# Kernel optimization log

Measured on AMD Instinct MI355X. Metric: run time of the kernel, lower is better.

Reference implementation:

```python
import jax, jax.numpy as jnp
import numpy as np

N_NODES = 100000
N_EDGES = 3200000
IN_C, HID_C, OUT_C = 64, 64, 32


def setup_inputs() -> dict:
    key = jax.random.key(0)
    ks = jax.random.split(key, 8)
    x = jax.random.normal(ks[0], (N_NODES, IN_C), dtype=jnp.float32)
    edge_index = jax.random.randint(ks[1], (2, N_EDGES), 0, N_NODES, dtype=jnp.int64)
    s1 = 1.0 / np.sqrt(IN_C)
    s2 = 1.0 / np.sqrt(HID_C)
    W1l = jax.random.uniform(ks[2], (IN_C, HID_C), jnp.float32, -s1, s1)
    b1l = jnp.zeros((HID_C,), jnp.float32)
    W1r = jax.random.uniform(ks[3], (IN_C, HID_C), jnp.float32, -s1, s1)
    W2l = jax.random.uniform(ks[4], (HID_C, OUT_C), jnp.float32, -s2, s2)
    b2l = jnp.zeros((OUT_C,), jnp.float32)
    W2r = jax.random.uniform(ks[5], (HID_C, OUT_C), jnp.float32, -s2, s2)
    return {"x": x, "edge_index": edge_index, "W1l": W1l, "b1l": b1l,
            "W1r": W1r, "W2l": W2l, "b2l": b2l, "W2r": W2r}


def _sage_conv(x, src, dst, Wl, bl, Wr):
    # mean-aggregate source features onto destination nodes
    msg = x[src]                                              # [E, d] gather
    summed = jax.ops.segment_sum(msg, dst, num_segments=N_NODES)
    deg = jax.ops.segment_sum(jnp.ones((src.shape[0],), x.dtype), dst,
                              num_segments=N_NODES)
    agg = summed / jnp.maximum(deg, 1.0)[:, None]             # [N, d]
    return agg @ Wl + bl + x @ Wr                             # lin_l(agg)+lin_r(x)


def reference(x, edge_index, W1l, b1l, W1r, W2l, b2l, W2r):
    src, dst = edge_index[0], edge_index[1]
    h = jax.nn.relu(_sage_conv(x, src, dst, W1l, b1l, W1r))
    # dropout is identity in eval mode
    return _sage_conv(h, src, dst, W2l, b2l, W2r)
```

## Files before the change

### kernel.cpp

```cpp
#include <hip/hip_runtime.h>
#include <hip/hip_bf16.h>

#define N_NODES 100000
#define N_EDGES 3200000
#define NBKT 391
#define BKT_CAP 10240

typedef __hip_bfloat16 bf16;
typedef unsigned int uint;
typedef __attribute__((ext_vector_type(8))) short bf16x8;
typedef __attribute__((ext_vector_type(4))) float f32x4;

__device__ __forceinline__ float b2f(bf16 v) { return __bfloat162float(v); }

__device__ __forceinline__ float bits2f(unsigned short w) {
    union { unsigned short u; bf16 b; } c;
    c.u = w;
    return __bfloat162float(c.b);
}
__device__ __forceinline__ unsigned short f2bits(float f) {
    return (unsigned short)(__float_as_uint(f) >> 16);
}
__device__ __forceinline__ unsigned short f2bf_bits(float f) {
    bf16 b = __float2bfloat16(f);
    unsigned short u;
    __builtin_memcpy(&u, &b, 2);
    return u;
}

__device__ __forceinline__ int get_idx(const void* ei, long long pos, int is64) {
    if (is64) return (int)((const long long*)ei)[pos];
    return ((const int*)ei)[pos];
}
__device__ __forceinline__ float get_f(const void* p, long long pos, int isbf) {
    if (isbf) return b2f(((const bf16*)p)[pos]);
    return ((const float*)p)[pos];
}

__global__ void detect_kernel(const void* __restrict__ x,
                              const void* __restrict__ ei,
                              int* __restrict__ flags) {
    int lane = threadIdx.x;
    const unsigned short* xw = (const unsigned short*)x;
    float v = bits2f(xw[2 * lane]);
    bool plaus = (v == v) && fabsf(v) > 1e-3f && fabsf(v) < 1e2f;
    unsigned long long m1 = __ballot(plaus);
    const int* iw = (const int*)ei;
    bool z = (iw[2 * lane + 1] == 0);
    unsigned long long m2 = __ballot(z);
    if (lane == 0) {
        flags[0] = (__popcll(m1) >= 32) ? 1 : 0;
        flags[1] = (__popcll(m2) == 64) ? 1 : 0;
    }
}

__global__ __launch_bounds__(256) void transpose_kernel(
    const void* __restrict__ x, uint4* __restrict__ xt,
    const int* __restrict__ flags) {
    if (!flags[0]) return;
    int i = blockIdx.x * 256 + threadIdx.x;
    if (i >= N_NODES * 4) return;
    int node = i >> 2, cz = i & 3;
    const uint4* x4 = (const uint4*)x;
    uint4 a = x4[(long long)node * 8 + cz * 2];
    uint4 b = x4[(long long)node * 8 + cz * 2 + 1];
    long long o = (long long)cz * (N_NODES * 2) + (long long)node * 2;
    xt[o] = a;
    xt[o + 1] = b;
}

__global__ __launch_bounds__(256) void scatterA_kernel(
    const void* __restrict__ ei, int* __restrict__ bucket_cursor,
    uint* __restrict__ bucket_data, const int* __restrict__ flags) {
    __shared__ int lhist[NBKT];
    __shared__ int lbase[NBKT];
    int is64 = flags[1];
    int t = threadIdx.x;
    int chunk0 = blockIdx.x * 8192;
    int dreg[32];

    for (int i = t; i < NBKT; i += 256) lhist[i] = 0;
    __syncthreads();
#pragma unroll
    for (int j = 0; j < 32; j++) {
        int e = chunk0 + j * 256 + t;
        int d = -1;
        if (e < N_EDGES) {
            d = get_idx(ei, (long long)N_EDGES + e, is64);
            atomicAdd(&lhist[d >> 8], 1);
        }
        dreg[j] = d;
    }
    __syncthreads();
    for (int i = t; i < NBKT; i += 256) {
        int c = lhist[i];
        lbase[i] = c ? atomicAdd(&bucket_cursor[i], c) : 0;
        lhist[i] = 0;
    }
    __syncthreads();
#pragma unroll
    for (int j = 0; j < 32; j++) {
        int e = chunk0 + j * 256 + t;
        int d = dreg[j];
        if (d >= 0) {
            int s = get_idx(ei, e, is64);
            int b = d >> 8;
            int o = lbase[b] + atomicAdd(&lhist[b], 1);
            if (o < BKT_CAP)
                bucket_data[(long long)b * BKT_CAP + o] = ((uint)(d & 255) << 17) | (uint)s;
        }
    }
}

__global__ void scanBuckets_kernel(const int* __restrict__ cnt,
                                   int* __restrict__ base) {
    __shared__ int buf[512];
    int t = threadIdx.x;
    int v = (t < NBKT) ? cnt[t] : 0;
    buf[t] = v;
    __syncthreads();
    for (int off = 1; off < 512; off <<= 1) {
        int add = (t >= off) ? buf[t - off] : 0;
        __syncthreads();
        buf[t] += add;
        __syncthreads();
    }
    if (t < NBKT) base[t] = buf[t] - v;
}

__global__ __launch_bounds__(256) void csrB_kernel(
    const int* __restrict__ bucket_cnt, const int* __restrict__ bucket_base,
    const uint* __restrict__ bucket_data, int* __restrict__ csr_src,
    int* __restrict__ row_start) {
    __shared__ int lh[256];
    __shared__ int buf[256];
    int b = blockIdx.x;
    int t = threadIdx.x;
    int cnt = bucket_cnt[b];
    if (cnt > BKT_CAP) cnt = BKT_CAP;
    int base = bucket_base[b];
    const uint* bd = bucket_data + (long long)b * BKT_CAP;

    lh[t] = 0;
    __syncthreads();
    for (int i = t; i < cnt; i += 256) atomicAdd(&lh[bd[i] >> 17], 1);
    __syncthreads();
    int v = lh[t];
    buf[t] = v;
    __syncthreads();
    for (int off = 1; off < 256; off <<= 1) {
        int add = (t >= off) ? buf[t - off] : 0;
        __syncthreads();
        buf[t] += add;
        __syncthreads();
    }
    int excl = buf[t] - v;
    int g = (b << 8) + t;
    if (g < N_NODES) row_start[g] = base + excl;
    lh[t] = excl;
    __syncthreads();
    for (int i = t; i < cnt; i += 256) {
        uint e = bd[i];
        int o = atomicAdd(&lh[e >> 17], 1);
        csr_src[base + o] = (int)(e & 0x1FFFFu);
    }
    if (b == 0 && t == 0) row_start[N_NODES] = N_EDGES;
}

#define ACC8(acc, v, v2)                                                         \
    acc[0] += __uint_as_float((v).x << 16) + __uint_as_float((v2).x << 16);       \
    acc[1] += __uint_as_float((v).x & 0xffff0000u) + __uint_as_float((v2).x & 0xffff0000u); \
    acc[2] += __uint_as_float((v).y << 16) + __uint_as_float((v2).y << 16);       \
    acc[3] += __uint_as_float((v).y & 0xffff0000u) + __uint_as_float((v2).y & 0xffff0000u); \
    acc[4] += __uint_as_float((v).z << 16) + __uint_as_float((v2).z << 16);       \
    acc[5] += __uint_as_float((v).z & 0xffff0000u) + __uint_as_float((v2).z & 0xffff0000u); \
    acc[6] += __uint_as_float((v).w << 16) + __uint_as_float((v2).w << 16);       \
    acc[7] += __uint_as_float((v).w & 0xffff0000u) + __uint_as_float((v2).w & 0xffff0000u);

#define ACCF4(acc, v, v2)                                                        \
    acc[0] += __uint_as_float((v).x) + __uint_as_float((v2).x);                   \
    acc[1] += __uint_as_float((v).y) + __uint_as_float((v2).y);                   \
    acc[2] += __uint_as_float((v).z) + __uint_as_float((v2).z);                   \
    acc[3] += __uint_as_float((v).w) + __uint_as_float((v2).w);

__global__ __launch_bounds__(256) void gather1_kernel(
    const void* __restrict__ x, const uint4* __restrict__ xt,
    const int* __restrict__ row_start, const int* __restrict__ csr_src,
    bf16* __restrict__ aggbuf, const int* __restrict__ flags) {
    int isbf = flags[0];
    int t = threadIdx.x;
    int lane = t & 63;
    int w = t >> 6;
    int bid = blockIdx.x;

    if (isbf) {
        int cz = (bid & 7) >> 1;
        int wid = ((((bid >> 3) << 1) | (bid & 1)) << 2) + w;
        int nw = gridDim.x;
        int e32 = lane >> 1, q2 = lane & 1;
        const uint4* xs = xt + (long long)cz * (N_NODES * 2);
        for (int quad = wid; quad < N_NODES / 4; quad += nw) {
            int nb0 = quad * 4;
            int r0 = row_start[nb0], r1 = row_start[nb0 + 1],
                r2 = row_start[nb0 + 2], r3 = row_start[nb0 + 3],
                r4 = row_start[nb0 + 4];
            int d0 = r1 - r0, d1 = r2 - r1, d2 = r3 - r2, d3 = r4 - r3;
            int maxd = max(max(d0, d1), max(d2, d3));
            float a0[8] = {0,0,0,0,0,0,0,0}, a1[8] = {0,0,0,0,0,0,0,0};
            float a2[8] = {0,0,0,0,0,0,0,0}, a3[8] = {0,0,0,0,0,0,0,0};
            for (int off = 0; off < maxd; off += 64) {
                int iA = r0 + off + e32, iA2 = iA + 32;
                int iB = r1 + off + e32, iB2 = iB + 32;
                int iC = r2 + off + e32, iC2 = iC + 32;
                int iD = r3 + off + e32, iD2 = iD + 32;
                int sA  = (iA  < r1) ? csr_src[iA]  : -1;
                int sA2 = (iA2 < r1) ? csr_src[iA2] : -1;
                int sB  = (iB  < r2) ? csr_src[iB]  : -1;
                int sB2 = (iB2 < r2) ? csr_src[iB2] : -1;
                int sC  = (iC  < r3) ? csr_src[iC]  : -1;
                int sC2 = (iC2 < r3) ? csr_src[iC2] : -1;
                int sD  = (iD  < r4) ? csr_src[iD]  : -1;
                int sD2 = (iD2 < r4) ? csr_src[iD2] : -1;
                uint4 vA = {0,0,0,0}, vA2 = {0,0,0,0}, vB = {0,0,0,0}, vB2 = {0,0,0,0};
                uint4 vC = {0,0,0,0}, vC2 = {0,0,0,0}, vD = {0,0,0,0}, vD2 = {0,0,0,0};
                if (sA  >= 0) vA  = xs[(sA  << 1) + q2];
                if (sA2 >= 0) vA2 = xs[(sA2 << 1) + q2];
                if (sB  >= 0) vB  = xs[(sB  << 1) + q2];
                if (sB2 >= 0) vB2 = xs[(sB2 << 1) + q2];
                if (sC  >= 0) vC  = xs[(sC  << 1) + q2];
                if (sC2 >= 0) vC2 = xs[(sC2 << 1) + q2];
                if (sD  >= 0) vD  = xs[(sD  << 1) + q2];
                if (sD2 >= 0) vD2 = xs[(sD2 << 1) + q2];
                ACC8(a0, vA, vA2)
                ACC8(a1, vB, vB2)
                ACC8(a2, vC, vC2)
                ACC8(a3, vD, vD2)
            }
#pragma unroll
            for (int m = 2; m <= 32; m <<= 1)
#pragma unroll
                for (int k = 0; k < 8; k++) {
                    a0[k] += __shfl_xor(a0[k], m, 64);
                    a1[k] += __shfl_xor(a1[k], m, 64);
                    a2[k] += __shfl_xor(a2[k], m, 64);
                    a3[k] += __shfl_xor(a3[k], m, 64);
                }
            int c = lane & 15, nl = lane >> 4;
            int srcq = (lane >> 3) & 1;
            float v0 = 0, v1 = 0, v2 = 0, v3 = 0;
#pragma unroll
            for (int k = 0; k < 8; k++) {
                float t0 = __shfl(a0[k], srcq, 64);
                float t1 = __shfl(a1[k], srcq, 64);
                float t2 = __shfl(a2[k], srcq, 64);
                float t3 = __shfl(a3[k], srcq, 64);
                bool sel = (lane & 7) == k;
                v0 = sel ? t0 : v0;
                v1 = sel ? t1 : v1;
                v2 = sel ? t2 : v2;
                v3 = sel ? t3 : v3;
            }
            float val = (nl == 0) ? v0 : (nl == 1) ? v1 : (nl == 2) ? v2 : v3;
            int dd = (nl == 0) ? d0 : (nl == 1) ? d1 : (nl == 2) ? d2 : d3;
            val *= 1.0f / fmaxf((float)dd, 1.0f);
            aggbuf[(long long)(nb0 + nl) * 64 + cz * 16 + c] = __float2bfloat16(val);
        }
    } else {
        int gw = (bid * 256 + t) >> 6;
        int nwv = (gridDim.x * 256) >> 6;
        int e4 = lane >> 4, q16 = lane & 15;
        const uint4* xf = (const uint4*)x;
        for (int p = gw; p * 2 < N_NODES; p += nwv) {
            int na = p * 2, nb = p * 2 + 1;
            int sa = row_start[na], ea = row_start[na + 1];
            int sb = row_start[nb], eb = row_start[nb + 1];
            int da = ea - sa, db = eb - sb;
            int maxd = max(da, db);
            float accA[4] = {0, 0, 0, 0};
            float accB[4] = {0, 0, 0, 0};
            for (int off = 0; off < maxd; off += 16) {
                int iA0 = sa + off + e4, iA1 = iA0 + 4, iA2 = iA0 + 8, iA3 = iA0 + 12;
                int iB0 = sb + off + e4, iB1 = iB0 + 4, iB2 = iB0 + 8, iB3 = iB0 + 12;
                int sA0 = (iA0 < ea) ? csr_src[iA0] : -1;
                int sA1 = (iA1 < ea) ? csr_src[iA1] : -1;
                int sA2 = (iA2 < ea) ? csr_src[iA2] : -1;
                int sA3 = (iA3 < ea) ? csr_src[iA3] : -1;
                int sB0 = (iB0 < eb) ? csr_src[iB0] : -1;
                int sB1 = (iB1 < eb) ? csr_src[iB1] : -1;
                int sB2 = (iB2 < eb) ? csr_src[iB2] : -1;
                int sB3 = (iB3 < eb) ? csr_src[iB3] : -1;
                uint4 vA0 = {0,0,0,0}, vA1 = {0,0,0,0}, vA2 = {0,0,0,0}, vA3 = {0,0,0,0};
                uint4 vB0 = {0,0,0,0}, vB1 = {0,0,0,0}, vB2 = {0,0,0,0}, vB3 = {0,0,0,0};
                if (sA0 >= 0) vA0 = xf[sA0 * 16 + q16];
                if (sA1 >= 0) vA1 = xf[sA1 * 16 + q16];
                if (sA2 >= 0) vA2 = xf[sA2 * 16 + q16];
                if (sA3 >= 0) vA3 = xf[sA3 * 16 + q16];
                if (sB0 >= 0) vB0 = xf[sB0 * 16 + q16];
                if (sB1 >= 0) vB1 = xf[sB1 * 16 + q16];
                if (sB2 >= 0) vB2 = xf[sB2 * 16 + q16];
                if (sB3 >= 0) vB3 = xf[sB3 * 16 + q16];
                ACCF4(accA, vA0, vA1)
                ACCF4(accA, vA2, vA3)
                ACCF4(accB, vB0, vB1)
                ACCF4(accB, vB2, vB3)
            }
#pragma unroll
            for (int m = 16; m <= 32; m <<= 1)
#pragma unroll
                for (int k = 0; k < 4; k++) {
                    accA[k] += __shfl_xor(accA[k], m, 64);
                    accB[k] += __shfl_xor(accB[k], m, 64);
                }
            float avA = 0.0f, avB = 0.0f;
#pragma unroll
            for (int k = 0; k < 4; k++) {
                float vA = __shfl(accA[k], lane >> 2, 64);
                float vB = __shfl(accB[k], lane >> 2, 64);
                avA = ((lane & 3) == k) ? vA : avA;
                avB = ((lane & 3) == k) ? vB : avB;
            }
            avA *= 1.0f / fmaxf((float)da, 1.0f);
            avB *= 1.0f / fmaxf((float)db, 1.0f);
            aggbuf[(long long)na * 64 + lane] = __float2bfloat16(avA);
            aggbuf[(long long)nb * 64 + lane] = __float2bfloat16(avB);
        }
    }
}

__global__ __launch_bounds__(256) void gemm1_kernel(
    const void* __restrict__ x, const bf16* __restrict__ aggbuf,
    const void* __restrict__ W1l, const void* __restrict__ b1l,
    const void* __restrict__ W1r, const void* __restrict__ W2l,
    const void* __restrict__ b2l, const void* __restrict__ W2r,
    bf16* __restrict__ zbufT, bf16* __restrict__ rbufT,
    const int* __restrict__ flags) {
    __shared__ __align__(16) unsigned short sW1t[64][136];
    __shared__ __align__(16) unsigned short sA[64][136];
    __shared__ __align__(16) unsigned short sW2t[64][72];
    __shared__ __align__(16) unsigned short sH[64][72];
    __shared__ float sB1[64];
    __shared__ float sB2[32];

    int isbf = flags[0];
    int t = threadIdx.x;
    int n0 = blockIdx.x * 64;

    for (int i = t; i < 64 * 128; i += 256) {
        int n = i & 63, k = i >> 6;
        unsigned short v;
        if (isbf)
            v = (k < 64) ? ((const unsigned short*)W1l)[k * 64 + n]
                         : ((const unsigned short*)W1r)[(k - 64) * 64 + n];
        else
            v = f2bits((k < 64) ? ((const float*)W1l)[k * 64 + n]
                                : ((const float*)W1r)[(k - 64) * 64 + n]);
        sW1t[n][k] = v;
    }
    for (int i = t; i < 64 * 64; i += 256) {
        int n = i & 63, k = i >> 6;
        unsigned short v;
        if (isbf)
            v = (n < 32) ? ((const unsigned short*)W2l)[k * 32 + n]
                         : ((const unsigned short*)W2r)[k * 32 + (n - 32)];
        else
            v = f2bits((n < 32) ? ((const float*)W2l)[k * 32 + n]
                                : ((const float*)W2r)[k * 32 + (n - 32)]);
        sW2t[n][k] = v;
    }
    if (t < 64) sB1[t] = get_f(b1l, t, isbf);
    if (t < 32) sB2[t] = get_f(b2l, t, isbf);

    const uint4* ag4 = (const uint4*)aggbuf;
    if (isbf) {
        const uint4* x4 = (const uint4*)x;
        for (int i = t; i < 64 * 16; i += 256) {
            int m = i >> 4, c = i & 15;
            int nn = min(n0 + m, N_NODES - 1);
            uint4 v = (c < 8) ? ag4[(long long)nn * 8 + c]
                              : x4[(long long)nn * 8 + (c - 8)];
            *(uint4*)&sA[m][c * 8] = v;
        }
    } else {
        for (int i = t; i < 64 * 8; i += 256) {
            int m = i >> 3, c = i & 7;
            int nn = min(n0 + m, N_NODES - 1);
            *(uint4*)&sA[m][c * 8] = ag4[(long long)nn * 8 + c];
        }
        const float* xf = (const float*)x;
        for (int i = t; i < 64 * 64; i += 256) {
            int m = i >> 6, c = i & 63;
            int nn = min(n0 + m, N_NODES - 1);
            sA[m][64 + c] = f2bf_bits(xf[(long long)nn * 64 + c]);
        }
    }
    __syncthreads();

    int w = t >> 6, lane = t & 63;
    int mbase = w * 16;
    int q = lane >> 4, r15 = lane & 15;
    f32x4 acc1[4] = {{0,0,0,0},{0,0,0,0},{0,0,0,0},{0,0,0,0}};
#pragma unroll
    for (int ks = 0; ks < 4; ks++) {
        bf16x8 afrag = *(const bf16x8*)&sA[mbase + r15][ks * 32 + q * 8];
#pragma unroll
        for (int nt = 0; nt < 4; nt++) {
            bf16x8 bfrag = *(const bf16x8*)&sW1t[nt * 16 + r15][ks * 32 + q * 8];
            acc1[nt] = __builtin_amdgcn_mfma_f32_16x16x32_bf16(afrag, bfrag, acc1[nt], 0, 0, 0);
        }
    }
#pragma unroll
    for (int nt = 0; nt < 4; nt++) {
        int col = nt * 16 + r15;
        float bias = sB1[col];
#pragma unroll
        for (int rr = 0; rr < 4; rr++) {
            int m = mbase + q * 4 + rr;
            sH[m][col] = f2bf_bits(fmaxf(acc1[nt][rr] + bias, 0.0f));
        }
    }
    __syncthreads();

    f32x4 acc2[4] = {{0,0,0,0},{0,0,0,0},{0,0,0,0},{0,0,0,0}};
#pragma unroll
    for (int ks = 0; ks < 2; ks++) {
        bf16x8 afrag = *(const bf16x8*)&sH[mbase + r15][ks * 32 + q * 8];
#pragma unroll
        for (int nt = 0; nt < 4; nt++) {
            bf16x8 bfrag = *(const bf16x8*)&sW2t[nt * 16 + r15][ks * 32 + q * 8];
            acc2[nt] = __builtin_amdgcn_mfma_f32_16x16x32_bf16(afrag, bfrag, acc2[nt], 0, 0, 0);
        }
    }
#pragma unroll
    for (int nt = 0; nt < 4; nt++) {
        int col = nt * 16 + r15;
#pragma unroll
        for (int rr = 0; rr < 4; rr++) {
            int m = mbase + q * 4 + rr;
            int n = n0 + m;
            if (n < N_NODES) {
                float v = acc2[nt][rr];
                if (col < 32) {
                    zbufT[(long long)(col >> 4) * (N_NODES * 16) +
                          (long long)n * 16 + (col & 15)] = __float2bfloat16(v);
                } else {
                    int c2 = col - 32;
                    rbufT[(long long)(c2 >> 4) * (N_NODES * 16) +
                          (long long)n * 16 + (c2 & 15)] =
                        __float2bfloat16(v + sB2[c2]);
                }
            }
        }
    }
}

__global__ __launch_bounds__(256) void node2_kernel(
    const int* __restrict__ row_start, const int* __restrict__ csr_src,
    const bf16* __restrict__ zT, const bf16* __restrict__ rbufT,
    void* __restrict__ out, const int* __restrict__ flags) {
    int isbf = flags[0];
    int t = threadIdx.x;
    int lane = t & 63;
    int w = t >> 6;
    int bid = blockIdx.x;
    int cz = (bid & 7) >> 2;
    int wid = ((((bid >> 3) << 2) | (bid & 3)) << 2) + w;
    int nw = gridDim.x * 2;
    const uint4* zs = (const uint4*)zT + (long long)cz * (N_NODES * 2);
    const bf16* rs = rbufT + (long long)cz * (N_NODES * 16);

    int e32 = lane >> 1, q2 = lane & 1;
    for (int quad = wid; quad < N_NODES / 4; quad += nw) {
        int nb0 = quad * 4;
        int r0 = row_start[nb0], r1 = row_start[nb0 + 1],
            r2 = row_start[nb0 + 2], r3 = row_start[nb0 + 3],
            r4 = row_start[nb0 + 4];
        int d0 = r1 - r0, d1 = r2 - r1, d2 = r3 - r2, d3 = r4 - r3;
        int maxd = max(max(d0, d1), max(d2, d3));
        float a0[8] = {0,0,0,0,0,0,0,0}, a1[8] = {0,0,0,0,0,0,0,0};
        float a2[8] = {0,0,0,0,0,0,0,0}, a3[8] = {0,0,0,0,0,0,0,0};
        for (int off = 0; off < maxd; off += 64) {
            int iA = r0 + off + e32, iA2 = iA + 32;
            int iB = r1 + off + e32, iB2 = iB + 32;
            int iC = r2 + off + e32, iC2 = iC + 32;
            int iD = r3 + off + e32, iD2 = iD + 32;
            int sA  = (iA  < r1) ? csr_src[iA]  : -1;
            int sA2 = (iA2 < r1) ? csr_src[iA2] : -1;
            int sB  = (iB  < r2) ? csr_src[iB]  : -1;
            int sB2 = (iB2 < r2) ? csr_src[iB2] : -1;
            int sC  = (iC  < r3) ? csr_src[iC]  : -1;
            int sC2 = (iC2 < r3) ? csr_src[iC2] : -1;
            int sD  = (iD  < r4) ? csr_src[iD]  : -1;
            int sD2 = (iD2 < r4) ? csr_src[iD2] : -1;
            uint4 vA = {0,0,0,0}, vA2 = {0,0,0,0}, vB = {0,0,0,0}, vB2 = {0,0,0,0};
            uint4 vC = {0,0,0,0}, vC2 = {0,0,0,0}, vD = {0,0,0,0}, vD2 = {0,0,0,0};
            if (sA  >= 0) vA  = zs[(sA  << 1) + q2];
            if (sA2 >= 0) vA2 = zs[(sA2 << 1) + q2];
            if (sB  >= 0) vB  = zs[(sB  << 1) + q2];
            if (sB2 >= 0) vB2 = zs[(sB2 << 1) + q2];
            if (sC  >= 0) vC  = zs[(sC  << 1) + q2];
            if (sC2 >= 0) vC2 = zs[(sC2 << 1) + q2];
            if (sD  >= 0) vD  = zs[(sD  << 1) + q2];
            if (sD2 >= 0) vD2 = zs[(sD2 << 1) + q2];
            ACC8(a0, vA, vA2)
            ACC8(a1, vB, vB2)
            ACC8(a2, vC, vC2)
            ACC8(a3, vD, vD2)
        }
#pragma unroll
        for (int m = 2; m <= 32; m <<= 1)
#pragma unroll
            for (int k = 0; k < 8; k++) {
                a0[k] += __shfl_xor(a0[k], m, 64);
                a1[k] += __shfl_xor(a1[k], m, 64);
                a2[k] += __shfl_xor(a2[k], m, 64);
                a3[k] += __shfl_xor(a3[k], m, 64);
            }
        int c = lane & 15, nl = lane >> 4;
        int srcq = (lane >> 3) & 1;
        float v0 = 0, v1 = 0, v2 = 0, v3 = 0;
#pragma unroll
        for (int k = 0; k < 8; k++) {
            float t0 = __shfl(a0[k], srcq, 64);
            float t1 = __shfl(a1[k], srcq, 64);
            float t2 = __shfl(a2[k], srcq, 64);
            float t3 = __shfl(a3[k], srcq, 64);
            bool sel = (lane & 7) == k;
            v0 = sel ? t0 : v0;
            v1 = sel ? t1 : v1;
            v2 = sel ? t2 : v2;
            v3 = sel ? t3 : v3;
        }
        float val = (nl == 0) ? v0 : (nl == 1) ? v1 : (nl == 2) ? v2 : v3;
        int dd = (nl == 0) ? d0 : (nl == 1) ? d1 : (nl == 2) ? d2 : d3;
        int n = nb0 + nl;
        int ch = cz * 16 + c;
        float res = val * (1.0f / fmaxf((float)dd, 1.0f))
                  + b2f(rs[(long long)n * 16 + c]);
        if (isbf)
            ((bf16*)out)[(long long)n * 32 + ch] = __float2bfloat16(res);
        else
            ((float*)out)[(long long)n * 32 + ch] = res;
    }
}

extern "C" void kernel_launch(void* const* d_in, const int* in_sizes, int n_in,
                              void* d_out, int out_size, void* d_ws, size_t ws_size,
                              hipStream_t stream) {
    const void* x = d_in[0];
    const void* ei = d_in[1];
    const void* W1l = d_in[2];
    const void* b1l = d_in[3];
    const void* W1r = d_in[4];
    const void* W2l = d_in[5];
    const void* b2l = d_in[6];
    const void* W2r = d_in[7];

    char* ws = (char*)d_ws;
    uint* bucket_data = (uint*)ws;
    bf16* aggbuf = (bf16*)ws;
    int* csr_src = (int*)(ws + 16015424);
    int* row_start = (int*)(ws + 28815424);
    int* bucket_cursor = (int*)(ws + 29215488);
    int* bucket_base = (int*)(ws + 29217088);
    uint4* xt = (uint4*)(ws + 29218688);
    bf16* zbufT = (bf16*)(ws + 29218688);
    bf16* rbufT = (bf16*)(ws + 35618688);
    int* flags = (int*)(ws + 42018688);

    hipMemsetAsync(bucket_cursor, 0, NBKT * 4, stream);

    detect_kernel<<<1, 64, 0, stream>>>(x, ei, flags);
    transpose_kernel<<<1563, 256, 0, stream>>>(x, xt, flags);
    scatterA_kernel<<<NBKT, 256, 0, stream>>>(ei, bucket_cursor, bucket_data, flags);
    scanBuckets_kernel<<<1, 512, 0, stream>>>(bucket_cursor, bucket_base);
    csrB_kernel<<<NBKT, 256, 0, stream>>>(bucket_cursor, bucket_base, bucket_data,
                                          csr_src, row_start);
    gather1_kernel<<<4096, 256, 0, stream>>>(x, xt, row_start, csr_src, aggbuf,
                                             flags);
    gemm1_kernel<<<1563, 256, 0, stream>>>(x, aggbuf, W1l, b1l, W1r, W2l, b2l,
                                           W2r, zbufT, rbufT, flags);
    node2_kernel<<<4096, 256, 0, stream>>>(row_start, csr_src, zbufT, rbufT,
                                           d_out, flags);
}
```

Measured before the change: 441.2 us.

## Restructure neighbor gather so each 8-lane group owns one node and channel slice

```diff
diff --git a/kernel.cpp b/kernel.cpp
--- a/kernel.cpp
+++ b/kernel.cpp
@@ -27,6 +27,8 @@
     __builtin_memcpy(&u, &b, 2);
     return u;
 }
+__device__ __forceinline__ float lo16f(uint w) { return __uint_as_float(w << 16); }
+__device__ __forceinline__ float hi16f(uint w) { return __uint_as_float(w & 0xffff0000u); }
 
 __device__ __forceinline__ int get_idx(const void* ei, long long pos, int is64) {
     if (is64) return (int)((const long long*)ei)[pos];
@@ -167,24 +169,51 @@
     if (b == 0 && t == 0) row_start[N_NODES] = N_EDGES;
 }
 
-#define ACC8(acc, v, v2)                                                         \
-    acc[0] += __uint_as_float((v).x << 16) + __uint_as_float((v2).x << 16);       \
-    acc[1] += __uint_as_float((v).x & 0xffff0000u) + __uint_as_float((v2).x & 0xffff0000u); \
-    acc[2] += __uint_as_float((v).y << 16) + __uint_as_float((v2).y << 16);       \
-    acc[3] += __uint_as_float((v).y & 0xffff0000u) + __uint_as_float((v2).y & 0xffff0000u); \
-    acc[4] += __uint_as_float((v).z << 16) + __uint_as_float((v2).z << 16);       \
-    acc[5] += __uint_as_float((v).z & 0xffff0000u) + __uint_as_float((v2).z & 0xffff0000u); \
-    acc[6] += __uint_as_float((v).w << 16) + __uint_as_float((v2).w << 16);       \
-    acc[7] += __uint_as_float((v).w & 0xffff0000u) + __uint_as_float((v2).w & 0xffff0000u);
-
 #define ACCF4(acc, v, v2)                                                        \
     acc[0] += __uint_as_float((v).x) + __uint_as_float((v2).x);                   \
     acc[1] += __uint_as_float((v).y) + __uint_as_float((v2).y);                   \
     acc[2] += __uint_as_float((v).z) + __uint_as_float((v2).z);                   \
     acc[3] += __uint_as_float((v).w) + __uint_as_float((v2).w);
 
+__device__ __forceinline__ void slice_gather8(
+    const uint* __restrict__ su, const int* __restrict__ row_start,
+    const int* __restrict__ csr_src, int nb0, int g8, int c8, int lane,
+    float& a0, float& a1, int& dg_out) {
+    int rl = (lane <= 8) ? row_start[nb0 + lane] : 0;
+    int sg = __shfl(rl, g8 >> 3, 64);
+    int eg = __shfl(rl, (g8 >> 3) + 1, 64);
+    int dg = eg - sg;
+    int maxd = dg;
+    maxd = max(maxd, __shfl_xor(maxd, 8, 64));
+    maxd = max(maxd, __shfl_xor(maxd, 16, 64));
+    maxd = max(maxd, __shfl_xor(maxd, 32, 64));
+
+    float s0f = 0.0f, s1f = 0.0f;
+    for (int base = 0; base < maxd; base += 8) {
+        int pf = sg + base + c8;
+        int sreg = (pf < eg) ? csr_src[pf] : 0;
+#pragma unroll
+        for (int u = 0; u < 8; u += 4) {
+            int s0 = __shfl(sreg, g8 + u, 64);
+            int s1 = __shfl(sreg, g8 + u + 1, 64);
+            int s2 = __shfl(sreg, g8 + u + 2, 64);
+            int s3 = __shfl(sreg, g8 + u + 3, 64);
+            uint w0 = 0, w1 = 0, w2 = 0, w3 = 0;
+            if (base + u < dg)     w0 = su[(s0 << 3) + c8];
+            if (base + u + 1 < dg) w1 = su[(s1 << 3) + c8];
+            if (base + u + 2 < dg) w2 = su[(s2 << 3) + c8];
+            if (base + u + 3 < dg) w3 = su[(s3 << 3) + c8];
+            s0f += lo16f(w0) + lo16f(w1) + lo16f(w2) + lo16f(w3);
+            s1f += hi16f(w0) + hi16f(w1) + hi16f(w2) + hi16f(w3);
+        }
+    }
+    a0 = s0f;
+    a1 = s1f;
+    dg_out = dg;
+}
+
 __global__ __launch_bounds__(256) void gather1_kernel(
-    const void* __restrict__ x, const uint4* __restrict__ xt,
+    const void* __restrict__ x, const uint* __restrict__ xtu,
     const int* __restrict__ row_start, const int* __restrict__ csr_src,
     bf16* __restrict__ aggbuf, const int* __restrict__ flags) {
     int isbf = flags[0];
@@ -197,73 +226,18 @@
         int cz = (bid & 7) >> 1;
         int wid = ((((bid >> 3) << 1) | (bid & 1)) << 2) + w;
         int nw = gridDim.x;
-        int e32 = lane >> 1, q2 = lane & 1;
-        const uint4* xs = xt + (long long)cz * (N_NODES * 2);
-        for (int quad = wid; quad < N_NODES / 4; quad += nw) {
-            int nb0 = quad * 4;
-            int r0 = row_start[nb0], r1 = row_start[nb0 + 1],
-                r2 = row_start[nb0 + 2], r3 = row_start[nb0 + 3],
-                r4 = row_start[nb0 + 4];
-            int d0 = r1 - r0, d1 = r2 - r1, d2 = r3 - r2, d3 = r4 - r3;
-            int maxd = max(max(d0, d1), max(d2, d3));
-            float a0[8] = {0,0,0,0,0,0,0,0}, a1[8] = {0,0,0,0,0,0,0,0};
-            float a2[8] = {0,0,0,0,0,0,0,0}, a3[8] = {0,0,0,0,0,0,0,0};
-            for (int off = 0; off < maxd; off += 64) {
-                int iA = r0 + off + e32, iA2 = iA + 32;
-                int iB = r1 + off + e32, iB2 = iB + 32;
-                int iC = r2 + off + e32, iC2 = iC + 32;
-                int iD = r3 + off + e32, iD2 = iD + 32;
-                int sA  = (iA  < r1) ? csr_src[iA]  : -1;
-                int sA2 = (iA2 < r1) ? csr_src[iA2] : -1;
-                int sB  = (iB  < r2) ? csr_src[iB]  : -1;
-                int sB2 = (iB2 < r2) ? csr_src[iB2] : -1;
-                int sC  = (iC  < r3) ? csr_src[iC]  : -1;
-                int sC2 = (iC2 < r3) ? csr_src[iC2] : -1;
-                int sD  = (iD  < r4) ? csr_src[iD]  : -1;
-                int sD2 = (iD2 < r4) ? csr_src[iD2] : -1;
-                uint4 vA = {0,0,0,0}, vA2 = {0,0,0,0}, vB = {0,0,0,0}, vB2 = {0,0,0,0};
-                uint4 vC = {0,0,0,0}, vC2 = {0,0,0,0}, vD = {0,0,0,0}, vD2 = {0,0,0,0};
-                if (sA  >= 0) vA  = xs[(sA  << 1) + q2];
-                if (sA2 >= 0) vA2 = xs[(sA2 << 1) + q2];
-                if (sB  >= 0) vB  = xs[(sB  << 1) + q2];
-                if (sB2 >= 0) vB2 = xs[(sB2 << 1) + q2];
-                if (sC  >= 0) vC  = xs[(sC  << 1) + q2];
-                if (sC2 >= 0) vC2 = xs[(sC2 << 1) + q2];
-                if (sD  >= 0) vD  = xs[(sD  << 1) + q2];
-                if (sD2 >= 0) vD2 = xs[(sD2 << 1) + q2];
-                ACC8(a0, vA, vA2)
-                ACC8(a1, vB, vB2)
-                ACC8(a2, vC, vC2)
-                ACC8(a3, vD, vD2)
-            }
-#pragma unroll
-            for (int m = 2; m <= 32; m <<= 1)
-#pragma unroll
-                for (int k = 0; k < 8; k++) {
-                    a0[k] += __shfl_xor(a0[k], m, 64);
-                    a1[k] += __shfl_xor(a1[k], m, 64);
-                    a2[k] += __shfl_xor(a2[k], m, 64);
-                    a3[k] += __shfl_xor(a3[k], m, 64);
-                }
-            int c = lane & 15, nl = lane >> 4;
-            int srcq = (lane >> 3) & 1;
-            float v0 = 0, v1 = 0, v2 = 0, v3 = 0;
-#pragma unroll
-            for (int k = 0; k < 8; k++) {
-                float t0 = __shfl(a0[k], srcq, 64);
-                float t1 = __shfl(a1[k], srcq, 64);
-                float t2 = __shfl(a2[k], srcq, 64);
-                float t3 = __shfl(a3[k], srcq, 64);
-                bool sel = (lane & 7) == k;
-                v0 = sel ? t0 : v0;
-                v1 = sel ? t1 : v1;
-                v2 = sel ? t2 : v2;
-                v3 = sel ? t3 : v3;
-            }
-            float val = (nl == 0) ? v0 : (nl == 1) ? v1 : (nl == 2) ? v2 : v3;
-            int dd = (nl == 0) ? d0 : (nl == 1) ? d1 : (nl == 2) ? d2 : d3;
-            val *= 1.0f / fmaxf((float)dd, 1.0f);
-            aggbuf[(long long)(nb0 + nl) * 64 + cz * 16 + c] = __float2bfloat16(val);
+        int g8 = lane & 0x38, c8 = lane & 7;
+        int g = lane >> 3;
+        const uint* su = xtu + (long long)cz * (N_NODES * 8);
+        uint* ag = (uint*)aggbuf;
+        for (int oct = wid; oct < N_NODES / 8; oct += nw) {
+            int nb0 = oct * 8;
+            float a0, a1;
+            int dg;
+            slice_gather8(su, row_start, csr_src, nb0, g8, c8, lane, a0, a1, dg);
+            float inv = 1.0f / fmaxf((float)dg, 1.0f);
+            uint pk = (uint)f2bf_bits(a0 * inv) | ((uint)f2bf_bits(a1 * inv) << 16);
+            ag[(nb0 + g) * 32 + cz * 8 + c8] = pk;
         }
     } else {
         int gw = (bid * 256 + t) >> 6;
@@ -455,7 +429,7 @@
 
 __global__ __launch_bounds__(256) void node2_kernel(
     const int* __restrict__ row_start, const int* __restrict__ csr_src,
-    const bf16* __restrict__ zT, const bf16* __restrict__ rbufT,
+    const uint* __restrict__ zTu, const bf16* __restrict__ rbufT,
     void* __restrict__ out, const int* __restrict__ flags) {
     int isbf = flags[0];
     int t = threadIdx.x;
@@ -465,81 +439,28 @@
     int cz = (bid & 7) >> 2;
     int wid = ((((bid >> 3) << 2) | (bid & 3)) << 2) + w;
     int nw = gridDim.x * 2;
-    const uint4* zs = (const uint4*)zT + (long long)cz * (N_NODES * 2);
-    const bf16* rs = rbufT + (long long)cz * (N_NODES * 16);
-
-    int e32 = lane >> 1, q2 = lane & 1;
-    for (int quad = wid; quad < N_NODES / 4; quad += nw) {
-        int nb0 = quad * 4;
-        int r0 = row_start[nb0], r1 = row_start[nb0 + 1],
-            r2 = row_start[nb0 + 2], r3 = row_start[nb0 + 3],
-            r4 = row_start[nb0 + 4];
-        int d0 = r1 - r0, d1 = r2 - r1, d2 = r3 - r2, d3 = r4 - r3;
-        int maxd = max(max(d0, d1), max(d2, d3));
-        float a0[8] = {0,0,0,0,0,0,0,0}, a1[8] = {0,0,0,0,0,0,0,0};
-        float a2[8] = {0,0,0,0,0,0,0,0}, a3[8] = {0,0,0,0,0,0,0,0};
-        for (int off = 0; off < maxd; off += 64) {
-            int iA = r0 + off + e32, iA2 = iA + 32;
-            int iB = r1 + off + e32, iB2 = iB + 32;
-            int iC = r2 + off + e32, iC2 = iC + 32;
-            int iD = r3 + off + e32, iD2 = iD + 32;
-            int sA  = (iA  < r1) ? csr_src[iA]  : -1;
-            int sA2 = (iA2 < r1) ? csr_src[iA2] : -1;
-            int sB  = (iB  < r2) ? csr_src[iB]  : -1;
-            int sB2 = (iB2 < r2) ? csr_src[iB2] : -1;
-            int sC  = (iC  < r3) ? csr_src[iC]  : -1;
-            int sC2 = (iC2 < r3) ? csr_src[iC2] : -1;
-            int sD  = (iD  < r4) ? csr_src[iD]  : -1;
-            int sD2 = (iD2 < r4) ? csr_src[iD2] : -1;
-            uint4 vA = {0,0,0,0}, vA2 = {0,0,0,0}, vB = {0,0,0,0}, vB2 = {0,0,0,0};
-            uint4 vC = {0,0,0,0}, vC2 = {0,0,0,0}, vD = {0,0,0,0}, vD2 = {0,0,0,0};
-            if (sA  >= 0) vA  = zs[(sA  << 1) + q2];
-            if (sA2 >= 0) vA2 = zs[(sA2 << 1) + q2];
-            if (sB  >= 0) vB  = zs[(sB  << 1) + q2];
-            if (sB2 >= 0) vB2 = zs[(sB2 << 1) + q2];
-            if (sC  >= 0) vC  = zs[(sC  << 1) + q2];
-            if (sC2 >= 0) vC2 = zs[(sC2 << 1) + q2];
-            if (sD  >= 0) vD  = zs[(sD  << 1) + q2];
-            if (sD2 >= 0) vD2 = zs[(sD2 << 1) + q2];
-            ACC8(a0, vA, vA2)
-            ACC8(a1, vB, vB2)
-            ACC8(a2, vC, vC2)
-            ACC8(a3, vD, vD2)
-        }
-#pragma unroll
-        for (int m = 2; m <= 32; m <<= 1)
-#pragma unroll
-            for (int k = 0; k < 8; k++) {
-                a0[k] += __shfl_xor(a0[k], m, 64);
-                a1[k] += __shfl_xor(a1[k], m, 64);
-                a2[k] += __shfl_xor(a2[k], m, 64);
-                a3[k] += __shfl_xor(a3[k], m, 64);
-            }
-        int c = lane & 15, nl = lane >> 4;
-        int srcq = (lane >> 3) & 1;
-        float v0 = 0, v1 = 0, v2 = 0, v3 = 0;
-#pragma unroll
-        for (int k = 0; k < 8; k++) {
-            float t0 = __shfl(a0[k], srcq, 64);
-            float t1 = __shfl(a1[k], srcq, 64);
-            float t2 = __shfl(a2[k], srcq, 64);
-            float t3 = __shfl(a3[k], srcq, 64);
-            bool sel = (lane & 7) == k;
-            v0 = sel ? t0 : v0;
-            v1 = sel ? t1 : v1;
-            v2 = sel ? t2 : v2;
-            v3 = sel ? t3 : v3;
-        }
-        float val = (nl == 0) ? v0 : (nl == 1) ? v1 : (nl == 2) ? v2 : v3;
-        int dd = (nl == 0) ? d0 : (nl == 1) ? d1 : (nl == 2) ? d2 : d3;
-        int n = nb0 + nl;
-        int ch = cz * 16 + c;
-        float res = val * (1.0f / fmaxf((float)dd, 1.0f))
-                  + b2f(rs[(long long)n * 16 + c]);
-        if (isbf)
-            ((bf16*)out)[(long long)n * 32 + ch] = __float2bfloat16(res);
-        else
-            ((float*)out)[(long long)n * 32 + ch] = res;
+    int g8 = lane & 0x38, c8 = lane & 7;
+    int g = lane >> 3;
+    const uint* su = zTu + (long long)cz * (N_NODES * 8);
+    const uint* ru = (const uint*)(rbufT + (long long)cz * (N_NODES * 16));
+
+    for (int oct = wid; oct < N_NODES / 8; oct += nw) {
+        int nb0 = oct * 8;
+        float a0, a1;
+        int dg;
+        slice_gather8(su, row_start, csr_src, nb0, g8, c8, lane, a0, a1, dg);
+        float inv = 1.0f / fmaxf((float)dg, 1.0f);
+        int n = nb0 + g;
+        uint rb = ru[n * 8 + c8];
+        float r0 = a0 * inv + lo16f(rb);
+        float r1 = a1 * inv + hi16f(rb);
+        if (isbf) {
+            uint pk = (uint)f2bf_bits(r0) | ((uint)f2bf_bits(r1) << 16);
+            ((uint*)out)[n * 16 + cz * 8 + c8] = pk;
+        } else {
+            ((float*)out)[(long long)n * 32 + cz * 16 + 2 * c8] = r0;
+            ((float*)out)[(long long)n * 32 + cz * 16 + 2 * c8 + 1] = r1;
+        }
     }
 }
 
@@ -562,7 +483,7 @@
     int* row_start = (int*)(ws + 28815424);
     int* bucket_cursor = (int*)(ws + 29215488);
     int* bucket_base = (int*)(ws + 29217088);
-    uint4* xt = (uint4*)(ws + 29218688);
+    uint* xtu = (uint*)(ws + 29218688);
     bf16* zbufT = (bf16*)(ws + 29218688);
     bf16* rbufT = (bf16*)(ws + 35618688);
     int* flags = (int*)(ws + 42018688);
@@ -570,15 +491,15 @@
     hipMemsetAsync(bucket_cursor, 0, NBKT * 4, stream);
 
     detect_kernel<<<1, 64, 0, stream>>>(x, ei, flags);
-    transpose_kernel<<<1563, 256, 0, stream>>>(x, xt, flags);
+    transpose_kernel<<<1563, 256, 0, stream>>>(x, (uint4*)xtu, flags);
     scatterA_kernel<<<NBKT, 256, 0, stream>>>(ei, bucket_cursor, bucket_data, flags);
     scanBuckets_kernel<<<1, 512, 0, stream>>>(bucket_cursor, bucket_base);
     csrB_kernel<<<NBKT, 256, 0, stream>>>(bucket_cursor, bucket_base, bucket_data,
                                           csr_src, row_start);
-    gather1_kernel<<<4096, 256, 0, stream>>>(x, xt, row_start, csr_src, aggbuf,
+    gather1_kernel<<<4096, 256, 0, stream>>>(x, xtu, row_start, csr_src, aggbuf,
                                              flags);
     gemm1_kernel<<<1563, 256, 0, stream>>>(x, aggbuf, W1l, b1l, W1r, W2l, b2l,
                                            W2r, zbufT, rbufT, flags);
-    node2_kernel<<<4096, 256, 0, stream>>>(row_start, csr_src, zbufT, rbufT,
-                                           d_out, flags);
-}
+    node2_kernel<<<4096, 256, 0, stream>>>(row_start, csr_src, (const uint*)zbufT,
+                                           rbufT, d_out, flags);
+}
```

Result: faster. 374.4 us (-15.1%).
